# Optimization experiments

Measured on AMD Instinct MI355X. Metric: run time of the kernel, lower is better.

Reference implementation:

```python
import jax, jax.numpy as jnp
import numpy as np
from jax import lax

# VGG16 conv configuration: (in_ch, out_ch) for 13 3x3 convs, blocks [2,2,3,3,3]
CONV_CFG = [(3,64),(64,64),(64,128),(128,128),(128,256),(256,256),(256,256),(256,512),(512,512),(512,512),(512,512),(512,512),(512,512)]
FC_CFG = [(512*7*7,4096),(4096,4096),(4096,1000)]
BLOCKS = [2,2,3,3,3]

def setup_inputs() -> dict:
    key = jax.random.key(0)
    ks = jax.random.split(key, 40)
    d = {"x": jax.random.normal(ks[0], (16,3,224,224), jnp.float32)}
    for i, (cin, cout) in enumerate(CONV_CFG):
        std = (2.0 / (cin * 9)) ** 0.5  # He init keeps 13-deep ReLU chain stable
        d[f"w{i+1}"] = jax.random.normal(ks[1+i], (cout, cin, 3, 3), jnp.float32) * std
        d[f"b{i+1}"] = jnp.zeros((cout,), jnp.float32)
    for j, (fin, fout) in enumerate(FC_CFG):
        std = (2.0 / fin) ** 0.5
        d[f"fw{j+1}"] = jax.random.normal(ks[20+j], (fin, fout), jnp.float32) * std
        d[f"fb{j+1}"] = jnp.zeros((fout,), jnp.float32)
    d["patch_location_tensor"] = jax.random.randint(ks[30], (16, 2), 0, 200)
    d["p_height"] = 16
    d["p_width"] = 16
    return d

def _conv_relu(x, w, b):
    # 3x3 conv, stride 1, SAME padding (pad=1), NCHW, followed by ReLU
    y = lax.conv_general_dilated(x, w, (1, 1), 'SAME', dimension_numbers=('NCHW', 'OIHW', 'NCHW'))
    return jax.nn.relu(y + b[None, :, None, None])

def _maxpool2(x):
    return lax.reduce_window(x, -jnp.inf, lax.max, (1, 1, 2, 2), (1, 1, 2, 2), 'VALID')

def reference(x, w1, b1, w2, b2, w3, b3, w4, b4, w5, b5, w6, b6, w7, b7, w8, b8, w9, b9, w10, b10, w11, b11, w12, b12, w13, b13, fw1, fb1, fw2, fb2, fw3, fb3, patch_location_tensor, p_height, p_width):
    # The incremental modules patch-update cached full-model activations; the net
    # result equals a dense VGG16 forward on x. patch_location_tensor / p_height /
    # p_width only control which region is recomputed, not the output values.
    ws = [w1, w2, w3, w4, w5, w6, w7, w8, w9, w10, w11, w12, w13]
    bs = [b1, b2, b3, b4, b5, b6, b7, b8, b9, b10, b11, b12, b13]
    h = x
    k = 0
    for n in BLOCKS:
        for _ in range(n):
            h = _conv_relu(h, ws[k], bs[k])
            k += 1
        h = _maxpool2(h)
    h = h.reshape(h.shape[0], -1)  # [B, 25088]
    h = jax.nn.relu(h @ fw1 + fb1)
    h = jax.nn.relu(h @ fw2 + fb2)
    return h @ fw3 + fb3  # [B, 1000]
```

## Files before the change

### kernel.cpp

```cpp
#include <hip/hip_runtime.h>
#include <hip/hip_bf16.h>

typedef __hip_bfloat16 bf16;
typedef __attribute__((ext_vector_type(4))) short s16x4;
typedef __attribute__((ext_vector_type(8))) short short8;
typedef __attribute__((ext_vector_type(8))) __bf16 bf16x8;
typedef __attribute__((ext_vector_type(4))) float f32x4;

__device__ __forceinline__ float s2f(short s) {
  return __builtin_bit_cast(float, (unsigned)((unsigned short)s) << 16);
}
__device__ __forceinline__ short f2s(float f) {
  return __builtin_bit_cast(short, __float2bfloat16(f));
}

__device__ __forceinline__ void gl16(const bf16* g, bf16* l) {
  __builtin_amdgcn_global_load_lds(
      (const __attribute__((address_space(1))) void*)g,
      (__attribute__((address_space(3))) void*)l, 16, 0, 0);
}

__global__ void zerofill(float* p, int n) {
  int i = blockIdx.x * 256 + threadIdx.x;
  if (i < n) p[i] = 0.f;
}

__global__ __launch_bounds__(256) void conv1_first(
    const float* __restrict__ x, const float* __restrict__ w,
    const float* __restrict__ b, bf16* __restrict__ out) {
  __shared__ float it[3][18][18];
  __shared__ float wl2[27 * 64];
  __shared__ float bl[64];
  const int tid = threadIdx.x;
  const int n = blockIdx.z;
  const int h0 = blockIdx.y * 16, w0 = blockIdx.x * 16;
  for (int i = tid; i < 1728; i += 256) {
    int jj = i >> 6, co = i & 63;
    wl2[i] = w[co * 27 + jj];
  }
  if (tid < 64) bl[tid] = b[tid];
  for (int i = tid; i < 972; i += 256) {
    int ci = i / 324; int r = i - ci * 324; int ty = r / 18, tx = r - ty * 18;
    int hh = h0 - 1 + ty, ww = w0 - 1 + tx;
    float v = 0.f;
    if (hh >= 0 && hh < 224 && ww >= 0 && ww < 224)
      v = x[((long)n * 3 + ci) * 50176 + hh * 224 + ww];
    it[ci][ty][tx] = v;
  }
  __syncthreads();
  const int ty = tid >> 4, tx = tid & 15;
  long ob = (((long)n * 224 + h0 + ty) * 224 + (w0 + tx)) * 64;
  for (int cog = 0; cog < 4; ++cog) {
    f32x4 a4[4];
    #pragma unroll
    for (int q = 0; q < 4; ++q) a4[q] = *(const f32x4*)&bl[cog * 16 + q * 4];
    #pragma unroll
    for (int jj = 0; jj < 27; ++jj) {
      const int ci = jj / 9, r = jj - ci * 9, kh = r / 3, kw = r - kh * 3;
      float v = it[ci][ty + kh][tx + kw];
      const f32x4* wp4 = (const f32x4*)&wl2[jj * 64 + cog * 16];
      #pragma unroll
      for (int q = 0; q < 4; ++q) a4[q] += v * wp4[q];
    }
    short8 s0, s1;
    #pragma unroll
    for (int u = 0; u < 4; ++u) {
      s0[u] = f2s(fmaxf(a4[0][u], 0.f));
      s0[4 + u] = f2s(fmaxf(a4[1][u], 0.f));
      s1[u] = f2s(fmaxf(a4[2][u], 0.f));
      s1[4 + u] = f2s(fmaxf(a4[3][u], 0.f));
    }
    *(short8*)(out + ob + cog * 16) = s0;
    *(short8*)(out + ob + cog * 16 + 8) = s1;
  }
}

struct RepackMeta {
  const float* src[12];
  long dstOff[12];
  int cinM1[12];
  int cshift[12];
  int cout[12];
};

__global__ __launch_bounds__(256) void repack_all(RepackMeta m, bf16* __restrict__ blob) {
  const int li = blockIdx.y;
  const int co = blockIdx.x;
  if (co >= m.cout[li]) return;
  const int cs = m.cshift[li];
  const int cinM1 = m.cinM1[li];
  const int K = 9 << cs;
  const float* src = m.src[li] + (long)co * (cinM1 + 1) * 9;
  bf16* dst = blob + m.dstOff[li] + (long)co * K;
  for (int k = threadIdx.x; k < K; k += 256) {
    int pos = k >> cs;
    int ci = k & cinM1;
    dst[k] = __float2bfloat16(src[ci * 9 + pos]);
  }
}

__global__ __launch_bounds__(256) void conv_halo64(
    const bf16* __restrict__ in, const bf16* __restrict__ wp,
    const float* __restrict__ bias, bf16* __restrict__ out,
    const bf16* __restrict__ zp) {
  __shared__ bf16 tA[10 * 34 * 64];
  __shared__ bf16 tB[9 * 64 * 64];
  const int tid = threadIdx.x;
  const int lane = tid & 63, wv = tid >> 6;
  const int n = blockIdx.z;
  const int h0 = blockIdx.y * 8, w0 = blockIdx.x * 32;

  #pragma unroll
  for (int i = 0; i < 11; ++i) {
    int cid = i * 256 + tid;
    if (cid < 2720) {
      int row = cid / 272;
      int rem = cid - row * 272;
      int w = rem >> 3, j = rem & 7;
      int hg = h0 - 1 + row, wg = w0 - 1 + w;
      bool ok = (hg >= 0) & (hg < 224) & (wg >= 0) & (wg < 224);
      const bf16* src = ok ? (in + (((long)n * 224 + hg) * 224 + wg) * 64 + ((j ^ (w & 7)) << 3))
                           : zp;
      gl16(src, tA + (long)cid * 8);
    }
  }
  {
    const int colB = tid >> 3;
    const int colx = ((tid & 7) ^ (colB & 7)) * 8;
    const bf16* s0 = wp + (long)colB * 576 + colx;
    const bf16* s1 = wp + (long)(colB + 32) * 576 + colx;
    #pragma unroll
    for (int p = 0; p < 9; ++p) {
      gl16(s0 + p * 64, tB + p * 4096 + tid * 8);
      gl16(s1 + p * 64, tB + p * 4096 + 2048 + tid * 8);
    }
  }
  __syncthreads();

  f32x4 acc[4][4];
  #pragma unroll
  for (int m = 0; m < 4; ++m)
    #pragma unroll
    for (int n2 = 0; n2 < 4; ++n2) acc[m][n2] = (f32x4){0.f, 0.f, 0.f, 0.f};

  for (int pos = 0; pos < 9; ++pos) {
    const int dh = pos / 3, dw = pos - (pos / 3) * 3;
    #pragma unroll
    for (int ks = 0; ks < 2; ++ks) {
      const int kb = ks * 64 + (lane >> 4) * 16;
      bf16x8 af[4], bfv[4];
      #pragma unroll
      for (int m = 0; m < 4; ++m) {
        int p = wv * 64 + m * 16 + (lane & 15);
        int hl = (p >> 5) + dh, wl = (p & 31) + dw;
        af[m] = *(const bf16x8*)((const char*)tA + hl * 4352 + wl * 128 + (kb ^ ((wl & 7) << 4)));
      }
      #pragma unroll
      for (int n2 = 0; n2 < 4; ++n2) {
        int c = n2 * 16 + (lane & 15);
        bfv[n2] = *(const bf16x8*)((const char*)tB + pos * 8192 + c * 128 + (kb ^ ((c & 7) << 4)));
      }
      #pragma unroll
      for (int m = 0; m < 4; ++m)
        #pragma unroll
        for (int n2 = 0; n2 < 4; ++n2)
          acc[m][n2] = __builtin_amdgcn_mfma_f32_16x16x32_bf16(af[m], bfv[n2], acc[m][n2], 0, 0, 0);
    }
  }

  const int ho = blockIdx.y * 4 + wv;
  #pragma unroll
  for (int m = 0; m < 2; ++m) {
    #pragma unroll
    for (int n2 = 0; n2 < 4; ++n2) {
      int co = n2 * 16 + (lane & 15);
      float bb = bias[co];
      #pragma unroll
      for (int qh = 0; qh < 2; ++qh) {
        int qq = 2 * qh;
        float v0 = fmaxf(acc[m][n2][qq] + bb, 0.f);
        float v1 = fmaxf(acc[m][n2][qq + 1] + bb, 0.f);
        float v2 = fmaxf(acc[m + 2][n2][qq] + bb, 0.f);
        float v3 = fmaxf(acc[m + 2][n2][qq + 1] + bb, 0.f);
        float mx = fmaxf(fmaxf(v0, v1), fmaxf(v2, v3));
        int wl = (m * 16 + ((lane >> 4) << 2) + qq) & 31;
        int wo = (w0 >> 1) + (wl >> 1);
        out[(((long)n * 112 + ho) * 112 + wo) * 64 + co] = __float2bfloat16(mx);
      }
    }
  }
}

template <int BM, int BN, int WM, int WN, int SPLITK>
__global__ __launch_bounds__(WM* WN * 64) void conv_gemm(
    const bf16* __restrict__ in, const bf16* __restrict__ wp,
    const float* __restrict__ bias, bf16* __restrict__ out,
    float* __restrict__ pout, const bf16* __restrict__ zp,
    int Cin, int cshift, int Cout, int H, int W, int NHW) {
  constexpr int NT = WM * WN * 64;
  constexpr int IA = BM * 8 / NT;
  constexpr int IB = BN * 8 / NT;
  __shared__ bf16 lA[BM * 64];
  __shared__ bf16 lB[BN * 64];
  const int tid = threadIdx.x;
  const int lane = tid & 63, wv = tid >> 6;
  const int wr = wv / WN, wc = wv % WN;

  const int gx = gridDim.x;
  const int nwg = gx * gridDim.y;
  const int fid = blockIdx.y * gx + blockIdx.x;
  const int q = nwg >> 3, r = nwg & 7;
  const int xcd = fid & 7, idx = fid >> 3;
  const int swz = (xcd < r ? xcd * (q + 1) : r * (q + 1) + (xcd - r) * q) + idx;
  const int p0 = (swz % gx) * BM;
  const int co0 = (swz / gx) * BN;

  const int K = 9 << cshift;
  const int HW = H * W;
  const int colx = ((tid & 7) ^ ((tid >> 3) & 7)) * 8;

  int baseA[IA]; short hA[IA], wA[IA];
  #pragma unroll
  for (int i = 0; i < IA; ++i) {
    int rr = i * (NT / 8) + (tid >> 3);
    int p = p0 + rr;
    if (p < NHW) {
      int n = p / HW; int rem = p - n * HW; int h = rem / W; int w_ = rem - h * W;
      hA[i] = (short)h; wA[i] = (short)w_;
      baseA[i] = ((n * H + h) * W + w_) * Cin;
    } else { hA[i] = -9999; wA[i] = -9999; baseA[i] = 0; }
  }

  f32x4 acc[4][4];
  #pragma unroll
  for (int m = 0; m < 4; ++m)
    #pragma unroll
    for (int n2 = 0; n2 < 4; ++n2) acc[m][n2] = (f32x4){0.f, 0.f, 0.f, 0.f};

  const int Kper = K / SPLITK;
  const int kBeg = (SPLITK > 1) ? (int)blockIdx.z * Kper : 0;
  const int kEnd = kBeg + Kper;

  const bf16* srcB[IB];
  #pragma unroll
  for (int i = 0; i < IB; ++i) {
    int col = i * (NT / 8) + (tid >> 3);
    srcB[i] = wp + (long)(co0 + col) * K + kBeg + colx;
  }

  int kk = kBeg;
  while (kk < kEnd) {
    const int pos = kk >> cshift;
    const int dh = pos / 3 - 1, dw = pos - (pos / 3) * 3 - 1;
    int posEnd = (pos + 1) << cshift;
    if (posEnd > kEnd) posEnd = kEnd;
    const bf16* srcA[IA];
    {
      const int doff = (dh * W + dw) * Cin + (kk & (Cin - 1)) + colx;
      #pragma unroll
      for (int i = 0; i < IA; ++i) {
        int hh = hA[i] + dh, ww = wA[i] + dw;
        bool ok = (hh >= 0) & (hh < H) & (ww >= 0) & (ww < W);
        srcA[i] = ok ? (in + baseA[i] + doff) : (zp + colx);
      }
    }
    for (; kk < posEnd; kk += 64) {
      __syncthreads();
      #pragma unroll
      for (int i = 0; i < IA; ++i) {
        gl16(srcA[i], lA + i * (NT * 8) + wv * 512);
        srcA[i] += 64;
      }
      #pragma unroll
      for (int i = 0; i < IB; ++i) {
        gl16(srcB[i], lB + i * (NT * 8) + wv * 512);
        srcB[i] += 64;
      }
      __syncthreads();
      #pragma unroll
      for (int ks = 0; ks < 2; ++ks) {
        const int kb = ks * 64 + (lane >> 4) * 16;
        bf16x8 af[4], bfv[4];
        #pragma unroll
        for (int m = 0; m < 4; ++m) {
          int rr = wr * 64 + m * 16 + (lane & 15);
          af[m] = *(const bf16x8*)((const char*)lA + rr * 128 + (kb ^ ((rr & 7) << 4)));
        }
        #pragma unroll
        for (int n2 = 0; n2 < 4; ++n2) {
          int c = wc * 64 + n2 * 16 + (lane & 15);
          bfv[n2] = *(const bf16x8*)((const char*)lB + c * 128 + (kb ^ ((c & 7) << 4)));
        }
        #pragma unroll
        for (int m = 0; m < 4; ++m)
          #pragma unroll
          for (int n2 = 0; n2 < 4; ++n2)
            acc[m][n2] = __builtin_amdgcn_mfma_f32_16x16x32_bf16(af[m], bfv[n2], acc[m][n2], 0, 0, 0);
      }
    }
  }

  if constexpr (SPLITK == 1) {
    #pragma unroll
    for (int m = 0; m < 4; ++m) {
      int pb = p0 + wr * 64 + m * 16 + (lane >> 4) * 4;
      #pragma unroll
      for (int n2 = 0; n2 < 4; ++n2) {
        int co = co0 + wc * 64 + n2 * 16 + (lane & 15);
        float bb = bias[co];
        #pragma unroll
        for (int qq = 0; qq < 4; ++qq) {
          int pp = pb + qq;
          if (pp < NHW)
            out[(long)pp * Cout + co] = __float2bfloat16(fmaxf(acc[m][n2][qq] + bb, 0.f));
        }
      }
    }
  } else {
    float* pb_ = pout + (long)blockIdx.z * NHW * Cout;
    #pragma unroll
    for (int m = 0; m < 4; ++m) {
      int pb = p0 + wr * 64 + m * 16 + (lane >> 4) * 4;
      #pragma unroll
      for (int n2 = 0; n2 < 4; ++n2) {
        int co = co0 + wc * 64 + n2 * 16 + (lane & 15);
        #pragma unroll
        for (int qq = 0; qq < 4; ++qq) {
          int pp = pb + qq;
          if (pp < NHW) pb_[(long)pp * Cout + co] = acc[m][n2][qq];
        }
      }
    }
  }
}

template <int NPARTS, bool POOL>
__global__ __launch_bounds__(256) void reduce_split(
    const float* __restrict__ part, const float* __restrict__ bias,
    bf16* __restrict__ out, int NHW, int H, int W, int C) {
  const long total = (long)NHW * C;
  if constexpr (!POOL) {
    long e4 = ((long)blockIdx.x * 256 + threadIdx.x) * 4;
    if (e4 >= total) return;
    f32x4 s = *(const f32x4*)(part + e4);
    #pragma unroll
    for (int p2 = 1; p2 < NPARTS; ++p2) {
      f32x4 b = *(const f32x4*)(part + (long)p2 * total + e4);
      s += b;
    }
    f32x4 bv = *(const f32x4*)(bias + (int)(e4 & (C - 1)));
    s16x4 r;
    #pragma unroll
    for (int u = 0; u < 4; ++u) r[u] = f2s(fmaxf(s[u] + bv[u], 0.f));
    *(s16x4*)(out + e4) = r;
  } else {
    const int H2 = H >> 1, W2 = W >> 1;
    long id4 = ((long)blockIdx.x * 256 + threadIdx.x) * 4;
    long ptotal = ((long)NHW / 4) * C;
    if (id4 >= ptotal) return;
    int c4 = (int)(id4 & (C - 1));
    long rest = id4 / C;
    int wo = (int)(rest % W2);
    long t2 = rest / W2;
    int ho = (int)(t2 % H2);
    int n = (int)(t2 / H2);
    f32x4 bv = *(const f32x4*)(bias + c4);
    f32x4 mx;
    #pragma unroll
    for (int dy = 0; dy < 2; ++dy)
      #pragma unroll
      for (int dx = 0; dx < 2; ++dx) {
        long p = ((long)n * H + 2 * ho + dy) * W + 2 * wo + dx;
        long e = p * C + c4;
        f32x4 s = *(const f32x4*)(part + e);
        #pragma unroll
        for (int p2 = 1; p2 < NPARTS; ++p2) {
          f32x4 b = *(const f32x4*)(part + (long)p2 * total + e);
          s += b;
        }
        s += bv;
        if (dy == 0 && dx == 0) mx = s;
        else {
          #pragma unroll
          for (int u = 0; u < 4; ++u) mx[u] = fmaxf(mx[u], s[u]);
        }
      }
    s16x4 r;
    #pragma unroll
    for (int u = 0; u < 4; ++u) r[u] = f2s(fmaxf(mx[u], 0.f));
    *(s16x4*)(out + ((long)(n * H2 + ho) * W2 + wo) * C + c4) = r;
  }
}

__global__ void maxpool_nhwc(const bf16* __restrict__ in, bf16* __restrict__ out,
                             int H, int W, int C, int cshift3, int WC8) {
  const int id = blockIdx.x * 256 + threadIdx.x;
  if (id >= WC8) return;
  const int H2 = H >> 1, W2 = W >> 1;
  const int ho = blockIdx.y, n = blockIdx.z;
  const int wo = id >> cshift3, c8 = id & ((1 << cshift3) - 1);
  const bf16* p = in + (((long)(n * H + 2 * ho) * W) + 2 * wo) * C + c8 * 8;
  short8 a = *(const short8*)p;
  short8 bq = *(const short8*)(p + C);
  short8 c = *(const short8*)(p + (long)W * C);
  short8 d = *(const short8*)(p + (long)W * C + C);
  short8 r;
  #pragma unroll
  for (int u = 0; u < 8; ++u) {
    float m = fmaxf(fmaxf(s2f(a[u]), s2f(bq[u])), fmaxf(s2f(c[u]), s2f(d[u])));
    r[u] = f2s(m);
  }
  *(short8*)(out + ((long)(n * H2 + ho) * W2 + wo) * C + c8 * 8) = r;
}

__global__ __launch_bounds__(256) void fc1_partial(
    const bf16* __restrict__ in, const float* __restrict__ w,
    float* __restrict__ part) {
  const int j0 = blockIdx.x * 1024 + threadIdx.x * 4;
  const int k0 = blockIdx.y * 128;
  __shared__ float ilds[128][16];
  #pragma unroll
  for (int i = 0; i < 8; ++i) {
    int e = i * 256 + threadIdx.x;
    int kk = e >> 4, n = e & 15;
    int k = k0 + kk;
    int cch = k / 49, s = k - cch * 49;
    ilds[kk][n] = s2f(__builtin_bit_cast(short, in[((long)n * 49 + s) * 512 + cch]));
  }
  __syncthreads();
  f32x4 acc[16];
  #pragma unroll
  for (int n = 0; n < 16; ++n) acc[n] = (f32x4){0.f, 0.f, 0.f, 0.f};
  #pragma unroll 4
  for (int kk = 0; kk < 128; ++kk) {
    f32x4 w4 = *(const f32x4*)(w + (long)(k0 + kk) * 4096 + j0);
    #pragma unroll
    for (int n = 0; n < 16; ++n) {
      float v = ilds[kk][n];
      acc[n] += v * w4;
    }
  }
  float* pp = part + (long)blockIdx.y * 16 * 4096;
  #pragma unroll
  for (int n = 0; n < 16; ++n) *(f32x4*)(pp + n * 4096 + j0) = acc[n];
}

template <int KPER>
__global__ __launch_bounds__(256) void fc23_partial(
    const float* __restrict__ in, const float* __restrict__ w,
    float* __restrict__ part, int fin, int fout) {
  const int j0 = blockIdx.x * 1024 + threadIdx.x * 4;
  const int k0 = blockIdx.y * KPER;
  __shared__ float ilds[KPER][16];
  #pragma unroll
  for (int i = 0; i < KPER / 16; ++i) {
    int e = i * 256 + threadIdx.x;
    int kk = e >> 4, n = e & 15;
    ilds[kk][n] = fmaxf(in[(long)n * fin + k0 + kk], 0.f);
  }
  __syncthreads();
  if (j0 >= fout) return;
  f32x4 acc[16];
  #pragma unroll
  for (int n = 0; n < 16; ++n) acc[n] = (f32x4){0.f, 0.f, 0.f, 0.f};
  #pragma unroll 4
  for (int kk = 0; kk < KPER; ++kk) {
    f32x4 w4 = *(const f32x4*)(w + (long)(k0 + kk) * fout + j0);
    #pragma unroll
    for (int n = 0; n < 16; ++n) {
      float v = ilds[kk][n];
      acc[n] += v * w4;
    }
  }
  float* pp = part + (long)blockIdx.y * 16 * fout;
  #pragma unroll
  for (int n = 0; n < 16; ++n) *(f32x4*)(pp + n * fout + j0) = acc[n];
}

__global__ void reduce_fc(const float* __restrict__ part, const float* __restrict__ bias,
                          float* __restrict__ out, int nparts, int fout, int total) {
  int i = blockIdx.x * 256 + threadIdx.x;
  if (i >= total) return;
  int n = i / fout, j = i - n * fout;
  float s = bias[j];
  for (int p = 0; p < nparts; ++p) s += part[((long)p * 16 + n) * fout + j];
  out[i] = s;
}

extern "C" void kernel_launch(void* const* d_in, const int* in_sizes, int n_in,
                              void* d_out, int out_size, void* d_ws, size_t ws_size,
                              hipStream_t stream) {
  const float* x = (const float*)d_in[0];
  const float* cw[13]; const float* cb[13];
  for (int i = 0; i < 13; ++i) { cw[i] = (const float*)d_in[1 + 2 * i]; cb[i] = (const float*)d_in[2 + 2 * i]; }
  const float* fw1 = (const float*)d_in[27]; const float* fb1 = (const float*)d_in[28];
  const float* fw2 = (const float*)d_in[29]; const float* fb2 = (const float*)d_in[30];
  const float* fw3 = (const float*)d_in[31]; const float* fb3 = (const float*)d_in[32];
  float* outp = (float*)d_out;

  const size_t REGION = 102760448;
  char* wsb = (char*)d_ws;
  bf16* A = (bf16*)wsb;
  bf16* B = (bf16*)(wsb + REGION);
  char* ST = wsb + 2 * REGION;
  bf16* zp = (bf16*)ST;
  bf16* WBLOB = (bf16*)(ST + 4096);
  char* ST2 = ST + 4096 + 31 * 1024 * 1024;
  float* F1 = (float*)ST2;
  float* F2 = F1 + 16 * 4096;
  float* PS = F2 + 16 * 4096;

  struct LayerCfg { int cin, cs, cout, H, W; };
  const LayerCfg L[12] = {
      {64, 6, 64, 224, 224},  {64, 6, 128, 112, 112}, {128, 7, 128, 112, 112},
      {128, 7, 256, 56, 56},  {256, 8, 256, 56, 56},  {256, 8, 256, 56, 56},
      {256, 8, 512, 28, 28},  {512, 9, 512, 28, 28},  {512, 9, 512, 28, 28},
      {512, 9, 512, 14, 14},  {512, 9, 512, 14, 14},  {512, 9, 512, 14, 14}};
  const bool poolAfter[12] = {true, false, true, false, false, true, false, false, true, false, false, true};

  RepackMeta rm;
  long off = 0;
  long offs[12];
  for (int li = 0; li < 12; ++li) {
    rm.src[li] = cw[li + 1];
    rm.cinM1[li] = L[li].cin - 1;
    rm.cshift[li] = L[li].cs;
    rm.cout[li] = L[li].cout;
    rm.dstOff[li] = off;
    offs[li] = off;
    off += (long)L[li].cout * (9 << L[li].cs);
  }
  zerofill<<<4, 256, 0, stream>>>((float*)zp, 1024);
  repack_all<<<dim3(512, 12), 256, 0, stream>>>(rm, WBLOB);

  conv1_first<<<dim3(14, 14, 16), 256, 0, stream>>>(x, cw[0], cb[0], A);

  bf16* cur = A;
  bf16* oth = B;
  for (int li = 0; li < 12; ++li) {
    const LayerCfg& c = L[li];
    bf16* wb = WBLOB + offs[li];
    const int NHW = 16 * c.H * c.W;
    const bool fusedPool = poolAfter[li] && (li == 0 || li >= 6);
    if (li == 0) {
      conv_halo64<<<dim3(7, 28, 16), 256, 0, stream>>>(cur, wb, cb[li + 1], oth, zp);
    } else if (li <= 2) {
      conv_gemm<256, 128, 4, 2, 1><<<dim3(NHW / 256, 1), 512, 0, stream>>>(
          cur, wb, cb[li + 1], oth, nullptr, zp, c.cin, c.cs, c.cout, c.H, c.W, NHW);
    } else if (li <= 5) {
      conv_gemm<128, 256, 2, 4, 1><<<dim3(NHW / 128, 1), 512, 0, stream>>>(
          cur, wb, cb[li + 1], oth, nullptr, zp, c.cin, c.cs, c.cout, c.H, c.W, NHW);
    } else if (li <= 8) {
      conv_gemm<128, 256, 2, 4, 2><<<dim3((NHW + 127) / 128, c.cout / 256, 2), 512, 0, stream>>>(
          cur, wb, cb[li + 1], nullptr, PS, zp, c.cin, c.cs, c.cout, c.H, c.W, NHW);
      if (fusedPool) {
        long pt = ((long)NHW / 4) * c.cout;
        reduce_split<2, true><<<(int)((pt / 4 + 255) / 256), 256, 0, stream>>>(
            PS, cb[li + 1], oth, NHW, c.H, c.W, c.cout);
      } else {
        long tot = (long)NHW * c.cout;
        reduce_split<2, false><<<(int)((tot / 4 + 255) / 256), 256, 0, stream>>>(
            PS, cb[li + 1], oth, NHW, c.H, c.W, c.cout);
      }
    } else {
      conv_gemm<128, 128, 2, 2, 4><<<dim3((NHW + 127) / 128, c.cout / 128, 4), 256, 0, stream>>>(
          cur, wb, cb[li + 1], nullptr, PS, zp, c.cin, c.cs, c.cout, c.H, c.W, NHW);
      if (fusedPool) {
        long pt = ((long)NHW / 4) * c.cout;
        reduce_split<4, true><<<(int)((pt / 4 + 255) / 256), 256, 0, stream>>>(
            PS, cb[li + 1], oth, NHW, c.H, c.W, c.cout);
      } else {
        long tot = (long)NHW * c.cout;
        reduce_split<4, false><<<(int)((tot / 4 + 255) / 256), 256, 0, stream>>>(
            PS, cb[li + 1], oth, NHW, c.H, c.W, c.cout);
      }
    }
    bf16* t = cur; cur = oth; oth = t;
    if (poolAfter[li] && !fusedPool) {
      int cs3 = (c.cout == 64) ? 3 : (c.cout == 128) ? 4 : (c.cout == 256) ? 5 : 6;
      int W2 = c.W / 2, H2 = c.H / 2;
      int WC8 = W2 << cs3;
      maxpool_nhwc<<<dim3((WC8 + 255) / 256, H2, 16), 256, 0, stream>>>(cur, oth, c.H, c.W, c.cout, cs3, WC8);
      t = cur; cur = oth; oth = t;
    }
  }
  float* P1 = (float*)oth;
  float* P2 = (float*)((char*)oth + 52u * 1024 * 1024);
  float* P3 = (float*)((char*)oth + 89u * 1024 * 1024);

  fc1_partial<<<dim3(4, 196), 256, 0, stream>>>(cur, fw1, P1);
  reduce_fc<<<(16 * 4096 + 255) / 256, 256, 0, stream>>>(P1, fb1, F1, 196, 4096, 16 * 4096);
  fc23_partial<32><<<dim3(4, 128), 256, 0, stream>>>(F1, fw2, P2, 4096, 4096);
  reduce_fc<<<(16 * 4096 + 255) / 256, 256, 0, stream>>>(P2, fb2, F2, 128, 4096, 16 * 4096);
  fc23_partial<32><<<dim3(1, 128), 256, 0, stream>>>(F2, fw3, P3, 4096, 1000);
  reduce_fc<<<(16 * 1000 + 255) / 256, 256, 0, stream>>>(P3, fb3, outp, 128, 1000, 16 * 1000);
}
```

Measured before the change: 1.061 ms.

## Add halo-tiled 128-channel conv kernel with fused maxpool for conv2_2

Adds a dedicated kernel for the second 128-channel conv at 112x112. It loads an 18x18x128 input halo tile into LDS once and reuses it across all nine filter taps, double-buffering the weight slices. Bias, ReLU and 2x2 maxpool are fused into the epilogue, so the full-resolution activation is never written and a separate pool pass is skipped. The cost is a large LDS footprint (about 146 KB per block), which limits occupancy, and a small grid of 784 blocks.

```diff
diff --git a/kernel.cpp b/kernel.cpp
--- a/kernel.cpp
+++ b/kernel.cpp
@@ -186,6 +186,108 @@
         int wl = (m * 16 + ((lane >> 4) << 2) + qq) & 31;
         int wo = (w0 >> 1) + (wl >> 1);
         out[(((long)n * 112 + ho) * 112 + wo) * 64 + co] = __float2bfloat16(mx);
+      }
+    }
+  }
+}
+
+__global__ __launch_bounds__(512) void conv_halo128p(
+    const bf16* __restrict__ in, const bf16* __restrict__ wp,
+    const float* __restrict__ bias, bf16* __restrict__ out,
+    const bf16* __restrict__ zp) {
+  __shared__ bf16 tA[18 * 18 * 128];
+  __shared__ bf16 tB[2][128 * 128];
+  const int tid = threadIdx.x;
+  const int lane = tid & 63, wv = tid >> 6;
+  const int wr = wv >> 1, wc = wv & 1;
+  const int n = blockIdx.z;
+  const int h0 = blockIdx.y * 16, w0 = blockIdx.x * 16;
+
+  #pragma unroll
+  for (int i = 0; i < 11; ++i) {
+    int cid = i * 512 + tid;
+    if (cid < 5184) {
+      int row = cid / 288;
+      int rem = cid - row * 288;
+      int w = rem >> 4, j = rem & 15;
+      int hg = h0 - 1 + row, wg = w0 - 1 + w;
+      bool ok = (hg >= 0) & (hg < 112) & (wg >= 0) & (wg < 112);
+      const bf16* src = ok ? (in + (((long)n * 112 + hg) * 112 + wg) * 128 + ((j ^ (w & 7)) << 3))
+                           : zp;
+      gl16(src, tA + (long)cid * 8);
+    }
+  }
+  #pragma unroll
+  for (int i = 0; i < 4; ++i) {
+    int cid = i * 512 + tid;
+    int co = cid >> 4, j = cid & 15;
+    const bf16* src = wp + (long)co * 1152 + ((j ^ (co & 7)) << 3);
+    gl16(src, tB[0] + (long)cid * 8);
+  }
+  __syncthreads();
+
+  f32x4 acc[4][4];
+  #pragma unroll
+  for (int m = 0; m < 4; ++m)
+    #pragma unroll
+    for (int n2 = 0; n2 < 4; ++n2) acc[m][n2] = (f32x4){0.f, 0.f, 0.f, 0.f};
+
+  for (int pos = 0; pos < 9; ++pos) {
+    if (pos < 8) {
+      bf16* dst = tB[(pos + 1) & 1];
+      #pragma unroll
+      for (int i = 0; i < 4; ++i) {
+        int cid = i * 512 + tid;
+        int co = cid >> 4, j = cid & 15;
+        const bf16* src = wp + (long)co * 1152 + (pos + 1) * 128 + ((j ^ (co & 7)) << 3);
+        gl16(src, dst + (long)cid * 8);
+      }
+    }
+    const bf16* bB = tB[pos & 1];
+    const int dh = pos / 3, dw = pos - (pos / 3) * 3;
+    #pragma unroll
+    for (int kq = 0; kq < 4; ++kq) {
+      const int kb = kq * 64 + (lane >> 4) * 16;
+      bf16x8 af[4], bfv[4];
+      #pragma unroll
+      for (int m = 0; m < 4; ++m) {
+        int hl = wr * 4 + m + dh;
+        int wl = (lane & 15) + dw;
+        af[m] = *(const bf16x8*)((const char*)tA + hl * 4608 + wl * 256 + (kb ^ ((wl & 7) << 4)));
+      }
+      #pragma unroll
+      for (int n2 = 0; n2 < 4; ++n2) {
+        int c = wc * 64 + n2 * 16 + (lane & 15);
+        bfv[n2] = *(const bf16x8*)((const char*)bB + c * 256 + (kb ^ ((c & 7) << 4)));
+      }
+      #pragma unroll
+      for (int m = 0; m < 4; ++m)
+        #pragma unroll
+        for (int n2 = 0; n2 < 4; ++n2)
+          acc[m][n2] = __builtin_amdgcn_mfma_f32_16x16x32_bf16(af[m], bfv[n2], acc[m][n2], 0, 0, 0);
+    }
+    __syncthreads();
+  }
+
+  const int hoB = blockIdx.y * 8, woB = blockIdx.x * 8;
+  #pragma unroll
+  for (int mh = 0; mh < 2; ++mh) {
+    const int m = 2 * mh;
+    const int ho = hoB + wr * 2 + mh;
+    #pragma unroll
+    for (int n2 = 0; n2 < 4; ++n2) {
+      int co = wc * 64 + n2 * 16 + (lane & 15);
+      float bb = bias[co];
+      #pragma unroll
+      for (int qh = 0; qh < 2; ++qh) {
+        int qq = 2 * qh;
+        float v0 = fmaxf(acc[m][n2][qq] + bb, 0.f);
+        float v1 = fmaxf(acc[m][n2][qq + 1] + bb, 0.f);
+        float v2 = fmaxf(acc[m + 1][n2][qq] + bb, 0.f);
+        float v3 = fmaxf(acc[m + 1][n2][qq + 1] + bb, 0.f);
+        float mx = fmaxf(fmaxf(v0, v1), fmaxf(v2, v3));
+        int wo = woB + (lane >> 4) * 2 + qh;
+        out[(((long)n * 56 + ho) * 56 + wo) * 128 + co] = __float2bfloat16(mx);
       }
     }
   }
@@ -541,12 +643,14 @@
     const LayerCfg& c = L[li];
     bf16* wb = WBLOB + offs[li];
     const int NHW = 16 * c.H * c.W;
-    const bool fusedPool = poolAfter[li] && (li == 0 || li >= 6);
+    const bool fusedPool = poolAfter[li] && (li == 0 || li == 2 || li >= 6);
     if (li == 0) {
       conv_halo64<<<dim3(7, 28, 16), 256, 0, stream>>>(cur, wb, cb[li + 1], oth, zp);
-    } else if (li <= 2) {
+    } else if (li == 1) {
       conv_gemm<256, 128, 4, 2, 1><<<dim3(NHW / 256, 1), 512, 0, stream>>>(
           cur, wb, cb[li + 1], oth, nullptr, zp, c.cin, c.cs, c.cout, c.H, c.W, NHW);
+    } else if (li == 2) {
+      conv_halo128p<<<dim3(7, 7, 16), 512, 0, stream>>>(cur, wb, cb[li + 1], oth, zp);
     } else if (li <= 5) {
       conv_gemm<128, 256, 2, 4, 1><<<dim3(NHW / 128, 1), 512, 0, stream>>>(
           cur, wb, cb[li + 1], oth, nullptr, zp, c.cin, c.cs, c.cout, c.H, c.W, NHW);
```

After: 1.018 ms. 4.1% less time.
